# Kernel optimization log

Measured on AMD Instinct MI355X. Metric: run time of the kernel, lower is better.

## Reference

```python
import jax, jax.numpy as jnp
import numpy as np

D = 512   # Nsites: single-particle Hilbert space dimension
N = 128   # Nparticles
TINY = 1e-30


def setup_inputs() -> dict:
    key = jax.random.key(0)
    k1, k2 = jax.random.split(key)
    # Orthonormal orbitals (mirrors reortho_orbitals: QR of a random matrix)
    A = jax.random.normal(k1, (D, D), dtype=jnp.float32)
    Q, _ = jnp.linalg.qr(A)
    P = Q[:, :N]                                   # (D, N) orthonormal columns
    u = jax.random.uniform(k2, (N,), dtype=jnp.float32)  # inverse-CDF draws, one per particle
    return {"P": P, "u": u}


def _sample(P, u):
    """Ordered componentwise sampling from the Slater determinant.

    Uses the identity that Ksites is always a contiguous range [0..i], so the
    determinant ratios -det(G[0:i+1]-diag(occ+e_i))/det(G[0:x_{k-1}+1]-diag(occ))
    reduce to running products of Schur-complement pivots s_j = G_jj - b^T Xinv b
    of the leading block of (G - diag(occ)).  A single O(D) scan maintains the
    (padded) inverse of that leading block via rank-1 bordered-inverse updates,
    replacing the per-step np.ix_/vstack/det kernel launches of the original.
    """
    dt = P.dtype
    G = jnp.eye(D, dtype=dt) - P @ P.T             # (D, D), symmetric projection complement
    idxs = jnp.arange(D)

    def step(carry, i):
        Xinv, ratio, cumul, k = carry
        b = jnp.where(idxs < i, G[:, i], 0.0)      # border column, masked to leading block
        v = Xinv @ b                               # Xinv is zero-padded beyond processed block
        s = G[i, i] - b @ v                        # Schur pivot (site i unoccupied)
        last_allowed = D - N + k                   # xmax - 1 for particle k
        active = (k < N) & (i <= last_allowed)
        # cond prob particle k sits at site i: -(s-1) * prod of unoccupied pivots since x_{k-1}
        p = jnp.where(active, -(s - 1.0) * ratio, 0.0)
        u_k = u[jnp.clip(k, 0, N - 1)]
        occupy = active & ((cumul + p >= u_k) | (i == last_allowed))  # inverse-CDF; force at support end
        pivot = jnp.where(occupy, s - 1.0, s)
        pivot = jnp.where(jnp.abs(pivot) < TINY, TINY, pivot)
        # bordered inverse update: [[X,b],[b,d]]^-1 via outer(vext,vext)/pivot
        vext = jnp.where(idxs == i, -1.0, v)
        Xinv = Xinv + jnp.outer(vext, vext) / pivot
        ratio = jnp.where(occupy, 1.0, jnp.where(active, ratio * s, ratio))
        cumul = jnp.where(occupy, 0.0, cumul + p)
        k = k + occupy.astype(jnp.int32)
        return (Xinv, ratio, cumul, k), (p, k - occupy.astype(jnp.int32), occupy)

    init = (jnp.zeros((D, D), dtype=dt), jnp.asarray(1.0, dt), jnp.asarray(0.0, dt),
            jnp.asarray(0, jnp.int32))
    _, (p_rec, k_rec, occ_rec) = jax.lax.scan(step, init, idxs)

    krow = jnp.where(k_rec < N, k_rec, N)          # out-of-range rows dropped
    cond_probs = jnp.zeros((N, D), dtype=dt).at[krow, idxs].set(p_rec, mode='drop')
    return cond_probs, occ_rec


def reference(P, u):
    cond_probs, occ = _sample(P, u)
    positions = jnp.nonzero(occ, size=N, fill_value=-1)[0]  # ordered sampled sites
    return cond_probs, positions
```

## Files before the change

### kernel.cpp

```cpp
#include <hip/hip_runtime.h>


#define DD 512
#define NN 128
#define NTHREADS 512
#define BB 16
#define NBLK (DD / BB)

__device__ __forceinline__ float lane_bcast(float v, int l) {
  return __int_as_float(__builtin_amdgcn_readlane(__float_as_int(v), l));
}

__device__ __forceinline__ float wave_reduce_add64(float sd) {
#if __has_builtin(__builtin_amdgcn_permlane32_swap)
  {
    unsigned xi = __float_as_uint(sd);
    auto r = __builtin_amdgcn_permlane32_swap(xi, xi, false, false);
    sd = __uint_as_float(r[0]) + __uint_as_float(r[1]);
  }
#else
  sd += __shfl_xor(sd, 32, 64);
#endif
#if __has_builtin(__builtin_amdgcn_permlane16_swap)
  {
    unsigned xi = __float_as_uint(sd);
    auto r = __builtin_amdgcn_permlane16_swap(xi, xi, false, false);
    sd = __uint_as_float(r[0]) + __uint_as_float(r[1]);
  }
#else
  sd += __shfl_xor(sd, 16, 64);
#endif
  sd += __int_as_float(
      __builtin_amdgcn_update_dpp(0, __float_as_int(sd), 0x128, 0xF, 0xF, true));
  sd += __int_as_float(
      __builtin_amdgcn_ds_swizzle(__float_as_int(sd), 0x101F));
  sd += __int_as_float(
      __builtin_amdgcn_update_dpp(0, __float_as_int(sd), 0x4E, 0xF, 0xF, true));
  sd += __int_as_float(
      __builtin_amdgcn_update_dpp(0, __float_as_int(sd), 0xB1, 0xF, 0xF, true));
  return sd;
}

__global__ __launch_bounds__(NTHREADS) void slater_scan_kernel(
    const float* __restrict__ P, const float* __restrict__ u,
    float* __restrict__ out) {
  const int tid   = threadIdx.x;
  const int wave  = tid >> 6;
  const int lane  = tid & 63;
  const int c0    = wave << 4;
  const int rbase = c0 & 63;
  const bool lowhalf = (wave < 4);

  __shared__ __align__(16) float part[8][64][36];
  __shared__ __align__(16) float Vld[128][20];
  __shared__ __align__(16) float Cld[16][20];

  for (int j = tid; j < NN * DD; j += NTHREADS) out[j] = 0.0f;

  const float ur0 = u[lane];
  const float ur1 = u[64 + lane];

  float A0[16], A1[16];
#pragma unroll
  for (int j = 0; j < 16; ++j) {
    A0[j] = (lane == c0 + j) ? 1.0f : 0.0f;
    A1[j] = (lane + 64 == c0 + j) ? 1.0f : 0.0f;
  }

  float ratio = 1.0f, cumul = 0.0f;
  int k = 0;

  __syncthreads();

  for (int blk = 0; blk < NBLK; ++blk) {
    const int i0 = blk * BB;

    float Pb0[16], Pb1[16];
    {
      const float* Pbase = P + i0 * NN + lane;
#pragma unroll
      for (int t = 0; t < 16; ++t) {
        Pb0[t] = Pbase[t * NN];
        Pb1[t] = Pbase[t * NN + 64];
      }
    }

    float pa0[16], pa1[16];
#pragma unroll
    for (int t = 0; t < 16; ++t) { pa0[t] = 0.0f; pa1[t] = 0.0f; }
    {
      auto body = [&](const float (&Pbh)[16]) {
#pragma unroll
        for (int j = 0; j < 16; ++j) {
          const float a0 = A0[j], a1 = A1[j];
#pragma unroll
          for (int t = 0; t < 16; ++t) {
            const float pcj = lane_bcast(Pbh[t], rbase + j);
            pa0[t] = fmaf(a0, pcj, pa0[t]);
            pa1[t] = fmaf(a1, pcj, pa1[t]);
          }
        }
      };
      if (lowhalf) body(Pb0); else body(Pb1);
    }
    {
      float4* myp = (float4*)&part[wave][lane][0];
      myp[0] = make_float4(pa0[0],  pa0[1],  pa0[2],  pa0[3]);
      myp[1] = make_float4(pa0[4],  pa0[5],  pa0[6],  pa0[7]);
      myp[2] = make_float4(pa0[8],  pa0[9],  pa0[10], pa0[11]);
      myp[3] = make_float4(pa0[12], pa0[13], pa0[14], pa0[15]);
      myp[4] = make_float4(pa1[0],  pa1[1],  pa1[2],  pa1[3]);
      myp[5] = make_float4(pa1[4],  pa1[5],  pa1[6],  pa1[7]);
      myp[6] = make_float4(pa1[8],  pa1[9],  pa1[10], pa1[11]);
      myp[7] = make_float4(pa1[12], pa1[13], pa1[14], pa1[15]);
    }
    __syncthreads();

    {
      const int r  = tid >> 2;
      const int qd = tid & 3;
      const int rl = r & 63;
      const int rh = (r >> 6) << 4;
      float s0 = 0.f, s1 = 0.f, s2 = 0.f, s3 = 0.f;
#pragma unroll
      for (int v = 0; v < 8; ++v) {
        const float4 x = *(const float4*)&part[v][rl][rh + 4 * qd];
        s0 += x.x; s1 += x.y; s2 += x.z; s3 += x.w;
      }
      *(float4*)&Vld[r][4 * qd] = make_float4(s0, s1, s2, s3);
    }
    __syncthreads();

    float W0[16], W1[16];
#pragma unroll
    for (int qd = 0; qd < 4; ++qd) {
      const float4 x = *(const float4*)&Vld[lane][4 * qd];
      W0[4 * qd + 0] = x.x; W0[4 * qd + 1] = x.y;
      W0[4 * qd + 2] = x.z; W0[4 * qd + 3] = x.w;
      const float4 y = *(const float4*)&Vld[lane + 64][4 * qd];
      W1[4 * qd + 0] = y.x; W1[4 * qd + 1] = y.y;
      W1[4 * qd + 2] = y.z; W1[4 * qd + 3] = y.w;
    }

    {
      float pt0l = 0.f, pt0h = 0.f, pt1l = 0.f, pt1h = 0.f;
#pragma unroll
      for (int j = 0; j < 16; j += 2) {
        const bool sel = (wave == (j >> 1));
        pt0l = sel ? Pb0[j]     : pt0l;  pt0h = sel ? Pb1[j]     : pt0h;
        pt1l = sel ? Pb0[j + 1] : pt1l;  pt1h = sel ? Pb1[j + 1] : pt1h;
      }
      float cr0[16], cr1[16];
#pragma unroll
      for (int mm = 0; mm < 16; ++mm) {
        cr0[mm] = wave_reduce_add64(fmaf(pt0l, W0[mm], pt0h * W1[mm]));
        cr1[mm] = wave_reduce_add64(fmaf(pt1l, W0[mm], pt1h * W1[mm]));
      }
      if (lane == 0) {
        float4* cp0 = (float4*)&Cld[2 * wave][0];
        cp0[0] = make_float4(cr0[0],  cr0[1],  cr0[2],  cr0[3]);
        cp0[1] = make_float4(cr0[4],  cr0[5],  cr0[6],  cr0[7]);
        cp0[2] = make_float4(cr0[8],  cr0[9],  cr0[10], cr0[11]);
        cp0[3] = make_float4(cr0[12], cr0[13], cr0[14], cr0[15]);
        float4* cp1 = (float4*)&Cld[2 * wave + 1][0];
        cp1[0] = make_float4(cr1[0],  cr1[1],  cr1[2],  cr1[3]);
        cp1[1] = make_float4(cr1[4],  cr1[5],  cr1[6],  cr1[7]);
        cp1[2] = make_float4(cr1[8],  cr1[9],  cr1[10], cr1[11]);
        cp1[3] = make_float4(cr1[12], cr1[13], cr1[14], cr1[15]);
      }
    }
    __syncthreads();

    const int m = lane & 15;
    float Cc[16];
#pragma unroll
    for (int t = 0; t < 16; ++t) Cc[t] = Cld[t][m];
    float qdiag = Cld[m][m];
    float Dreg[16];
    float invpv[16];
    bool done = false;
#pragma unroll
    for (int t = 0; t < 16; ++t) {
      const float s = 1.0f - lane_bcast(qdiag, t);
      const int i = i0 + t;
      const int last_allowed = DD - NN + k;
      const bool active = (k < NN) && (i <= last_allowed);
      const float pr = active ? (-(s - 1.0f) * ratio) : 0.0f;
      const int kidx = (k < NN) ? k : (NN - 1);
      const float uk_l = lane_bcast(ur0, kidx & 63);
      const float uk_h = lane_bcast(ur1, kidx & 63);
      const float uk = (kidx < 64) ? uk_l : uk_h;
      const bool occupy = active && ((cumul + pr >= uk) || (i == last_allowed));
      float pivot = occupy ? (s - 1.0f) : s;
      pivot = (fabsf(pivot) < 1e-30f) ? 1e-30f : pivot;
      const float invp = 1.0f / pivot;

      if (tid == 0) {
        if (k < NN) out[k * DD + i] = pr;
        if (occupy) out[NN * DD + k] = (float)i;
      }

      ratio = occupy ? 1.0f : (active ? ratio * s : ratio);
      cumul = occupy ? 0.0f : (cumul + pr);
      k += occupy ? 1 : 0;
      if (k == NN) { done = true; break; }

      float d = Cc[t];
#pragma unroll
      for (int j = 0; j < t; ++j) {
        const float f = lane_bcast(Dreg[j], t) * invpv[j];
        d     = fmaf(f, Dreg[j], d);
        W0[t] = fmaf(f, W0[j], W0[t]);
        W1[t] = fmaf(f, W1[j], W1[t]);
      }
      Dreg[t]  = d;
      invpv[t] = invp;
      qdiag = fmaf(d * invp, d, qdiag);
    }
    if (done) return;

    {
      float Ws0[16], Ws1[16];
#pragma unroll
      for (int t = 0; t < 16; ++t) {
        Ws0[t] = W0[t] * invpv[t];
        Ws1[t] = W1[t] * invpv[t];
      }
      auto upd = [&](const float (&Wh)[16]) {
#pragma unroll
        for (int j = 0; j < 16; ++j) {
#pragma unroll
          for (int t = 0; t < 16; ++t) {
            const float wc = lane_bcast(Wh[t], rbase + j);
            A0[j] = fmaf(Ws0[t], wc, A0[j]);
            A1[j] = fmaf(Ws1[t], wc, A1[j]);
          }
        }
      };
      if (lowhalf) upd(W0); else upd(W1);
    }
  }
}

extern "C" void kernel_launch(void* const* d_in, const int* in_sizes, int n_in,
                              void* d_out, int out_size, void* d_ws,
                              size_t ws_size, hipStream_t stream) {
  const float* P = (const float*)d_in[0];
  const float* u = (const float*)d_in[1];
  float* out = (float*)d_out;
  hipLaunchKernelGGL(slater_scan_kernel, dim3(1), dim3(NTHREADS), 0, stream,
                     P, u, out);
}
```

Baseline: 488.0 us.

## Use packed FP32 FMAs with scalar operands for Xinv block products

```diff
diff --git a/kernel.cpp b/kernel.cpp
--- a/kernel.cpp
+++ b/kernel.cpp
@@ -7,8 +7,19 @@
 #define BB 16
 #define NBLK (DD / BB)
 
+typedef float v2f __attribute__((ext_vector_type(2)));
+
 __device__ __forceinline__ float lane_bcast(float v, int l) {
   return __int_as_float(__builtin_amdgcn_readlane(__float_as_int(v), l));
+}
+
+__device__ __forceinline__ void pk_fma_vs(v2f& acc, v2f a, v2f bs) {
+  asm("v_pk_fma_f32 %0, %1, %2, %0" : "+v"(acc) : "v"(a), "s"(bs));
+}
+__device__ __forceinline__ v2f pk_mul_vs(v2f a, v2f bs) {
+  v2f d;
+  asm("v_pk_mul_f32 %0, %1, %2" : "=v"(d) : "v"(a), "s"(bs));
+  return d;
 }
 
 __device__ __forceinline__ float wave_reduce_add64(float sd) {
@@ -60,11 +71,13 @@
   const float ur0 = u[lane];
   const float ur1 = u[64 + lane];
 
-  float A0[16], A1[16];
-#pragma unroll
-  for (int j = 0; j < 16; ++j) {
-    A0[j] = (lane == c0 + j) ? 1.0f : 0.0f;
-    A1[j] = (lane + 64 == c0 + j) ? 1.0f : 0.0f;
+  v2f A2r0[8], A2r1[8];
+#pragma unroll
+  for (int jp = 0; jp < 8; ++jp) {
+    A2r0[jp] = (v2f){(lane == c0 + 2 * jp) ? 1.0f : 0.0f,
+                     (lane == c0 + 2 * jp + 1) ? 1.0f : 0.0f};
+    A2r1[jp] = (v2f){(lane + 64 == c0 + 2 * jp) ? 1.0f : 0.0f,
+                     (lane + 64 == c0 + 2 * jp + 1) ? 1.0f : 0.0f};
   }
 
   float ratio = 1.0f, cumul = 0.0f;
@@ -74,34 +87,29 @@
 
   for (int blk = 0; blk < NBLK; ++blk) {
     const int i0 = blk * BB;
-
-    float Pb0[16], Pb1[16];
-    {
-      const float* Pbase = P + i0 * NN + lane;
-#pragma unroll
-      for (int t = 0; t < 16; ++t) {
-        Pb0[t] = Pbase[t * NN];
-        Pb1[t] = Pbase[t * NN + 64];
-      }
-    }
+    const int c0u = __builtin_amdgcn_readfirstlane(c0);
+    const float* Pu = P + i0 * NN + c0u;
+
+    const int tr = i0 + 2 * wave;
+    const float pt0l = P[tr * NN + lane];
+    const float pt0h = P[tr * NN + 64 + lane];
+    const float pt1l = P[tr * NN + NN + lane];
+    const float pt1h = P[tr * NN + NN + 64 + lane];
 
     float pa0[16], pa1[16];
 #pragma unroll
-    for (int t = 0; t < 16; ++t) { pa0[t] = 0.0f; pa1[t] = 0.0f; }
-    {
-      auto body = [&](const float (&Pbh)[16]) {
-#pragma unroll
-        for (int j = 0; j < 16; ++j) {
-          const float a0 = A0[j], a1 = A1[j];
-#pragma unroll
-          for (int t = 0; t < 16; ++t) {
-            const float pcj = lane_bcast(Pbh[t], rbase + j);
-            pa0[t] = fmaf(a0, pcj, pa0[t]);
-            pa1[t] = fmaf(a1, pcj, pa1[t]);
-          }
-        }
-      };
-      if (lowhalf) body(Pb0); else body(Pb1);
+    for (int t = 0; t < 16; ++t) {
+      const v2f* pr2 = (const v2f*)(Pu + t * NN);
+      v2f a0 = pk_mul_vs(A2r0[0], pr2[0]);
+      v2f a1 = pk_mul_vs(A2r1[0], pr2[0]);
+#pragma unroll
+      for (int jp = 1; jp < 8; ++jp) {
+        const v2f sp = pr2[jp];
+        pk_fma_vs(a0, A2r0[jp], sp);
+        pk_fma_vs(a1, A2r1[jp], sp);
+      }
+      pa0[t] = a0.x + a0.y;
+      pa1[t] = a1.x + a1.y;
     }
     {
       float4* myp = (float4*)&part[wave][lane][0];
@@ -143,13 +151,6 @@
     }
 
     {
-      float pt0l = 0.f, pt0h = 0.f, pt1l = 0.f, pt1h = 0.f;
-#pragma unroll
-      for (int j = 0; j < 16; j += 2) {
-        const bool sel = (wave == (j >> 1));
-        pt0l = sel ? Pb0[j]     : pt0l;  pt0h = sel ? Pb1[j]     : pt0h;
-        pt1l = sel ? Pb0[j + 1] : pt1l;  pt1h = sel ? Pb1[j + 1] : pt1h;
-      }
       float cr0[16], cr1[16];
 #pragma unroll
       for (int mm = 0; mm < 16; ++mm) {
@@ -176,8 +177,7 @@
 #pragma unroll
     for (int t = 0; t < 16; ++t) Cc[t] = Cld[t][m];
     float qdiag = Cld[m][m];
-    float Dreg[16];
-    float invpv[16];
+    float Dreg[16], SD[16], SW0[16], SW1[16];
     bool done = false;
 #pragma unroll
     for (int t = 0; t < 16; ++t) {
@@ -208,32 +208,31 @@
       float d = Cc[t];
 #pragma unroll
       for (int j = 0; j < t; ++j) {
-        const float f = lane_bcast(Dreg[j], t) * invpv[j];
-        d     = fmaf(f, Dreg[j], d);
-        W0[t] = fmaf(f, W0[j], W0[t]);
-        W1[t] = fmaf(f, W1[j], W1[t]);
-      }
-      Dreg[t]  = d;
-      invpv[t] = invp;
-      qdiag = fmaf(d * invp, d, qdiag);
+        const float djt = lane_bcast(Dreg[j], t);
+        d     = fmaf(djt, SD[j],  d);
+        W0[t] = fmaf(djt, SW0[j], W0[t]);
+        W1[t] = fmaf(djt, SW1[j], W1[t]);
+      }
+      Dreg[t] = d;
+      SD[t]   = d * invp;
+      SW0[t]  = W0[t] * invp;
+      SW1[t]  = W1[t] * invp;
+      qdiag   = fmaf(d, SD[t], qdiag);
     }
     if (done) return;
 
     {
-      float Ws0[16], Ws1[16];
-#pragma unroll
-      for (int t = 0; t < 16; ++t) {
-        Ws0[t] = W0[t] * invpv[t];
-        Ws1[t] = W1[t] * invpv[t];
-      }
       auto upd = [&](const float (&Wh)[16]) {
 #pragma unroll
-        for (int j = 0; j < 16; ++j) {
-#pragma unroll
-          for (int t = 0; t < 16; ++t) {
-            const float wc = lane_bcast(Wh[t], rbase + j);
-            A0[j] = fmaf(Ws0[t], wc, A0[j]);
-            A1[j] = fmaf(Ws1[t], wc, A1[j]);
+        for (int t = 0; t < 16; ++t) {
+          const v2f w0d = {SW0[t], SW0[t]};
+          const v2f w1d = {SW1[t], SW1[t]};
+#pragma unroll
+          for (int jp = 0; jp < 8; ++jp) {
+            const v2f wc2 = {lane_bcast(Wh[t], rbase + 2 * jp),
+                             lane_bcast(Wh[t], rbase + 2 * jp + 1)};
+            pk_fma_vs(A2r0[jp], w0d, wc2);
+            pk_fma_vs(A2r1[jp], w1d, wc2);
           }
         }
       };
```

Result: no change. 484.4 us (-0.7%).
